# Kernel optimization log

Hardware: AMD Instinct MI355X
Metric: run time of the kernel (lower is better)

Reference implementation:

```python
import jax, jax.numpy as jnp
import numpy as np

NUM_VARS = 64
LAG = 16
H1 = 64
H2 = 1024
NUM_OUT = 1
BATCH = 16384


def setup_inputs() -> dict:
    key = jax.random.key(0)
    ks = jax.random.split(key, 8)

    def xavier(k, shape, fan_in, fan_out):
        std = float(np.sqrt(2.0 / (fan_in + fan_out)))
        return jax.random.normal(k, shape, dtype=jnp.float32) * std

    inputs = jax.random.normal(ks[0], (BATCH, NUM_VARS * LAG), dtype=jnp.float32)
    # Per-variable sub-network weights, batched over the variable axis.
    W1 = xavier(ks[1], (NUM_VARS, LAG, H1), LAG, H1)
    b1 = jnp.full((NUM_VARS, H1), 0.1, dtype=jnp.float32)
    W2 = xavier(ks[2], (NUM_VARS, H1, H1), H1, H1)
    b2 = jnp.full((NUM_VARS, H1), 0.1, dtype=jnp.float32)
    imp = (jnp.ones((NUM_VARS,), dtype=jnp.float32) / NUM_VARS
           + 1e-5 * jax.random.normal(ks[3], (NUM_VARS,), dtype=jnp.float32))
    W3 = xavier(ks[4], (NUM_VARS * H1, H2), NUM_VARS * H1, H2)
    b3 = jnp.full((H2,), 0.1, dtype=jnp.float32)
    W4 = xavier(ks[5], (H2, NUM_OUT), H2, NUM_OUT)
    b4 = jnp.full((NUM_OUT,), 0.1, dtype=jnp.float32)
    return {"inputs": inputs, "W1": W1, "b1": b1, "W2": W2, "b2": b2,
            "imp": imp, "W3": W3, "b3": b3, "W4": W4, "b4": b4}


def reference(inputs, W1, b1, W2, b2, imp, W3, b3, W4, b4):
    B = inputs.shape[0]
    # [B, V*lag] -> [B, V, lag]; slicing inputs[:, lag*i:lag*(i+1)] == x[:, i, :]
    x = inputs.reshape(B, NUM_VARS, LAG)
    # dp = 0.0 -> dropout is identity
    h = jax.nn.relu(jnp.einsum('bvl,vlh->bvh', x, W1) + b1[None])      # [B, V, H1]
    h = jax.nn.relu(jnp.einsum('bvh,vhk->bvk', h, W2) + b2[None])      # [B, V, H1]
    agg = (h * imp[None, :, None]).reshape(B, NUM_VARS * H1)            # weighted concat
    pred = jax.nn.relu(agg @ W3 + b3) @ W4 + b4                        # [B, NUM_OUT]
    return pred
```

## Files before the change

kernel.cpp:

```cpp
#include <hip/hip_runtime.h>
#include <hip/hip_bf16.h>
#include <stdint.h>

#define B_ROWS 16384
#define NVARS 64
#define LAG 16
#define H1 64
#define H2 1024
#define KDIM (NVARS * H1)

typedef __attribute__((ext_vector_type(8))) short short8;
typedef __attribute__((ext_vector_type(4))) short short4v;
typedef __attribute__((ext_vector_type(4))) float f32x4;

typedef __attribute__((address_space(3))) uint8_t lds_u8;
typedef const __attribute__((address_space(1))) uint8_t glob_u8;

__device__ __forceinline__ void gload_lds16(const void* g, void* l) {
    __builtin_amdgcn_global_load_lds((glob_u8*)g, (lds_u8*)l, 16, 0, 0);
}

__device__ __forceinline__ short f2bf_s(float x) {
    __hip_bfloat16 h = __float2bfloat16(x);
    return *(short*)&h;
}
__device__ __forceinline__ float bf_s2f(short s) {
    __hip_bfloat16 h = *(__hip_bfloat16*)&s;
    return __bfloat162float(h);
}

__global__ __launch_bounds__(256) void prep_w12_kernel(
    const float* __restrict__ W1, const float* __restrict__ W2,
    short* __restrict__ w1bh, short* __restrict__ w1bl,
    short* __restrict__ w2bh, short* __restrict__ w2bl) {
    const int v = blockIdx.x, t = threadIdx.x;
    for (int idx = t; idx < 64 * 32; idx += 256) {
        int col = idx >> 5, k = idx & 31;
        float wv = W1[((size_t)v * LAG + (k & 15)) * H1 + col];
        short hi = f2bf_s(wv);
        w1bh[((size_t)v * 64 + col) * 40 + k] = hi;
        w1bl[((size_t)v * 64 + col) * 40 + k] = (k < 16) ? f2bf_s(wv - bf_s2f(hi)) : (short)0;
    }
    for (int idx = t; idx < 64 * 64; idx += 256) {
        int col = idx >> 6, k = idx & 63;
        float wv = W2[((size_t)v * H1 + k) * H1 + col];
        short hi = f2bf_s(wv);
        w2bh[((size_t)v * 64 + col) * 72 + k] = hi;
        w2bl[((size_t)v * 64 + col) * 72 + k] = f2bf_s(wv - bf_s2f(hi));
    }
}

__global__ __launch_bounds__(256) void subnets_fused_kernel(
    const float* __restrict__ inputs, const float* __restrict__ b1g,
    const float* __restrict__ b2g, const float* __restrict__ impg,
    const short* __restrict__ w1bh_g, const short* __restrict__ w1bl_g,
    const short* __restrict__ w2bh_g, const short* __restrict__ w2bl_g,
    const float* __restrict__ w3, const float* __restrict__ b4,
    __hip_bfloat16* __restrict__ w3t, float* __restrict__ out,
    __hip_bfloat16* __restrict__ agg) {
    __shared__ __align__(16) char smem[38912];
    const int bid = blockIdx.x;
    const int t = threadIdx.x;

    if (bid < 1024) {
        float (*tile)[65] = (float (*)[65])smem;
        const int k0 = (bid >> 4) * 64;
        const int n0 = (bid & 15) * 64;
        const int c = t & 63, r0 = t >> 6;
#pragma unroll
        for (int i = 0; i < 16; i++) {
            int r = r0 + i * 4;
            tile[r][c] = w3[(size_t)(k0 + r) * H2 + n0 + c];
        }
        __syncthreads();
#pragma unroll
        for (int i = 0; i < 16; i++) {
            int nr = r0 + i * 4;
            w3t[(size_t)(n0 + nr) * KDIM + k0 + c] = __float2bfloat16(tile[c][nr]);
        }
        return;
    }
    if (bid < 1088) {
        out[(bid - 1024) * 256 + t] = b4[0];
        return;
    }

    const int sbid = bid - 1088;
    const int v = sbid >> 7;
    const int b0 = (sbid & 127) * 128;
    const int lane = t & 63, wv = t >> 6;
    const int l15 = lane & 15, g = lane >> 4;

    short* xsS   = (short*)smem;
    short* w1bhS = (short*)(smem + 10240);
    short* w1blS = (short*)(smem + 15360);
    short* Hs    = (short*)smem;
    short* w2bhS = (short*)(smem + 20480);
    short* w2blS = (short*)(smem + 29696);

    for (int c = t; c < 320; c += 256) {
        gload_lds16(w1bh_g + (size_t)v * 2560 + c * 8, (char*)w1bhS + c * 16);
        gload_lds16(w1bl_g + (size_t)v * 2560 + c * 8, (char*)w1blS + c * 16);
    }
    for (int c = t; c < 576; c += 256) {
        gload_lds16(w2bh_g + (size_t)v * 4608 + c * 8, (char*)w2bhS + c * 16);
        gload_lds16(w2bl_g + (size_t)v * 4608 + c * 8, (char*)w2blS + c * 16);
    }
#pragma unroll
    for (int i = 0; i < 2; i++) {
        int idx = t + i * 256;
        int row = idx >> 2, seg = idx & 3;
        float4 x4 = *(const float4*)(inputs + (size_t)(b0 + row) * (NVARS * LAG) + v * LAG + seg * 4);
        const float* xp = (const float*)&x4;
        short4v hv, lv;
#pragma unroll
        for (int j = 0; j < 4; j++) {
            short hi = f2bf_s(xp[j]);
            hv[j] = hi;
            lv[j] = f2bf_s(xp[j] - bf_s2f(hi));
        }
        *(short4v*)&xsS[row * 40 + seg * 4] = hv;
        *(short4v*)&xsS[row * 40 + 16 + seg * 4] = lv;
    }
    __syncthreads();

    short8 a1[2], b1hF[4], b1lF[4];
#pragma unroll
    for (int mt = 0; mt < 2; mt++)
        a1[mt] = *(const short8*)&xsS[(wv * 32 + mt * 16 + l15) * 40 + g * 8];
#pragma unroll
    for (int nt = 0; nt < 4; nt++) {
        b1hF[nt] = *(const short8*)&w1bhS[(nt * 16 + l15) * 40 + g * 8];
        b1lF[nt] = *(const short8*)&w1blS[(nt * 16 + l15) * 40 + g * 8];
    }
    f32x4 acc1[2][4];
#pragma unroll
    for (int mt = 0; mt < 2; mt++)
#pragma unroll
        for (int nt = 0; nt < 4; nt++) {
            acc1[mt][nt] = (f32x4){0.f, 0.f, 0.f, 0.f};
            acc1[mt][nt] = __builtin_amdgcn_mfma_f32_16x16x32_bf16(a1[mt], b1hF[nt], acc1[mt][nt], 0, 0, 0);
            acc1[mt][nt] = __builtin_amdgcn_mfma_f32_16x16x32_bf16(a1[mt], b1lF[nt], acc1[mt][nt], 0, 0, 0);
        }
    __syncthreads();

#pragma unroll
    for (int mt = 0; mt < 2; mt++)
#pragma unroll
        for (int nt = 0; nt < 4; nt++) {
            int col = nt * 16 + l15;
            float bias = b1g[v * H1 + col];
#pragma unroll
            for (int r = 0; r < 4; r++) {
                float h = fmaxf(acc1[mt][nt][r] + bias, 0.f);
                int row = wv * 32 + mt * 16 + g * 4 + r;
                Hs[row * 72 + col] = f2bf_s(h);
            }
        }
    __syncthreads();

    short8 a2[2][2], b2hF[4][2], b2lF[4][2];
#pragma unroll
    for (int mt = 0; mt < 2; mt++)
#pragma unroll
        for (int kc = 0; kc < 2; kc++)
            a2[mt][kc] = *(const short8*)&Hs[(wv * 32 + mt * 16 + l15) * 72 + kc * 32 + g * 8];
#pragma unroll
    for (int nt = 0; nt < 4; nt++)
#pragma unroll
        for (int kc = 0; kc < 2; kc++) {
            b2hF[nt][kc] = *(const short8*)&w2bhS[(nt * 16 + l15) * 72 + kc * 32 + g * 8];
            b2lF[nt][kc] = *(const short8*)&w2blS[(nt * 16 + l15) * 72 + kc * 32 + g * 8];
        }
    f32x4 acc2[2][4];
#pragma unroll
    for (int mt = 0; mt < 2; mt++)
#pragma unroll
        for (int nt = 0; nt < 4; nt++) {
            f32x4 a = (f32x4){0.f, 0.f, 0.f, 0.f};
            a = __builtin_amdgcn_mfma_f32_16x16x32_bf16(a2[mt][0], b2hF[nt][0], a, 0, 0, 0);
            a = __builtin_amdgcn_mfma_f32_16x16x32_bf16(a2[mt][1], b2hF[nt][1], a, 0, 0, 0);
            a = __builtin_amdgcn_mfma_f32_16x16x32_bf16(a2[mt][0], b2lF[nt][0], a, 0, 0, 0);
            a = __builtin_amdgcn_mfma_f32_16x16x32_bf16(a2[mt][1], b2lF[nt][1], a, 0, 0, 0);
            acc2[mt][nt] = a;
        }

    const float impv = impg[v];
#pragma unroll
    for (int mt = 0; mt < 2; mt++)
#pragma unroll
        for (int nt = 0; nt < 4; nt++) {
            int col = nt * 16 + l15;
            float bias = b2g[v * H1 + col];
#pragma unroll
            for (int r = 0; r < 4; r++) {
                float o = fmaxf(acc2[mt][nt][r] + bias, 0.f) * impv;
                int row = b0 + wv * 32 + mt * 16 + g * 4 + r;
                agg[(size_t)row * KDIM + v * H1 + col] = __float2bfloat16(o);
            }
        }
}

#define NT 128

__global__ __launch_bounds__(512, 4) void gemm3_kernel(
    const __hip_bfloat16* __restrict__ agg,
    const __hip_bfloat16* __restrict__ w3t,
    const float* __restrict__ b3, const float* __restrict__ W4,
    float* __restrict__ out) {
    const int bid = ((blockIdx.x & 7) << 6) + (blockIdx.x >> 3);
    const int brow = (bid >> 2) * 128;
    const int bcol = (bid & 3) * 256;
    const int t = threadIdx.x;
    const int lane = t & 63;
    const int wid = t >> 6;
    const int wm = wid >> 2, wn = wid & 3;
    const int l15 = lane & 15, g = lane >> 4;

    __shared__ __align__(16) char smem[73728];

    const int rA = t >> 2;
    const int colA = ((t & 3) * 8) ^ ((rA & 8) ? 16 : 0);
    const int cB0 = t, cB1 = t + 512;
    const int rB0 = cB0 >> 2, rB1 = cB1 >> 2;
    const int colB0 = ((cB0 & 3) * 8) ^ ((rB0 & 8) ? 16 : 0);
    const int colB1 = ((cB1 & 3) * 8) ^ ((rB1 & 8) ? 16 : 0);
    const __hip_bfloat16* aS = agg + (size_t)(brow + rA) * KDIM + colA;
    const __hip_bfloat16* bS0 = w3t + (size_t)(bcol + rB0) * KDIM + colB0;
    const __hip_bfloat16* bS1 = w3t + (size_t)(bcol + rB1) * KDIM + colB1;

#define STAGE(p, kt) do { \
        gload_lds16(aS + (size_t)(kt) * 32,  smem + (p) * 24576 + t * 16); \
        gload_lds16(bS0 + (size_t)(kt) * 32, smem + (p) * 24576 + 8192 + cB0 * 16); \
        gload_lds16(bS1 + (size_t)(kt) * 32, smem + (p) * 24576 + 8192 + cB1 * 16); } while (0)

    const int coff = (g * 16) ^ ((l15 & 8) ? 32 : 0);
    const int aBase = (wm * 64 + l15) * 64 + coff;
    const int bBase = 8192 + (wn * 64 + l15) * 64 + coff;

#define LDFRAGS(p) do { \
        fa[0] = *(const short8*)(smem + (p) * 24576 + aBase + 0 * 1024); \
        fa[1] = *(const short8*)(smem + (p) * 24576 + aBase + 1 * 1024); \
        fa[2] = *(const short8*)(smem + (p) * 24576 + aBase + 2 * 1024); \
        fa[3] = *(const short8*)(smem + (p) * 24576 + aBase + 3 * 1024); \
        fb[0] = *(const short8*)(smem + (p) * 24576 + bBase + 0 * 1024); \
        fb[1] = *(const short8*)(smem + (p) * 24576 + bBase + 1 * 1024); \
        fb[2] = *(const short8*)(smem + (p) * 24576 + bBase + 2 * 1024); \
        fb[3] = *(const short8*)(smem + (p) * 24576 + bBase + 3 * 1024); } while (0)

#define MM() do { \
        __builtin_amdgcn_s_setprio(1); \
        _Pragma("unroll") \
        for (int mm = 0; mm < 4; mm++) \
            _Pragma("unroll") \
            for (int nn = 0; nn < 4; nn++) \
                acc[mm][nn] = __builtin_amdgcn_mfma_f32_16x16x32_bf16( \
                    fa[mm], fb[nn], acc[mm][nn], 0, 0, 0); \
        __builtin_amdgcn_s_setprio(0); } while (0)

#define TILE(p, DOSTAGE, ps, kts, VMSTR) do { \
        if (DOSTAGE) STAGE(ps, kts); \
        LDFRAGS(p); \
        MM(); \
        asm volatile(VMSTR ::: "memory"); \
        __builtin_amdgcn_s_barrier(); \
        __builtin_amdgcn_sched_barrier(0); } while (0)

    short8 fa[4], fb[4];
    f32x4 acc[4][4];
#pragma unroll
    for (int m = 0; m < 4; m++)
#pragma unroll
        for (int n = 0; n < 4; n++) acc[m][n] = (f32x4){0.f, 0.f, 0.f, 0.f};

    STAGE(0, 0);
    STAGE(1, 1);
    asm volatile("s_waitcnt vmcnt(3)" ::: "memory");
    __builtin_amdgcn_s_barrier();
    __builtin_amdgcn_sched_barrier(0);

    for (int i = 0; i < 42; ++i) {
        const int tt = i * 3;
        TILE(0, 1, 2, tt + 2, "s_waitcnt vmcnt(3)");
        TILE(1, 1, 0, tt + 3, "s_waitcnt vmcnt(3)");
        TILE(2, 1, 1, tt + 4, "s_waitcnt vmcnt(3)");
    }
    TILE(0, 0, 0, 0, "s_waitcnt vmcnt(0)");
    LDFRAGS(1);
    MM();

    float bias[4], w4v[4];
#pragma unroll
    for (int n = 0; n < 4; n++) {
        int col = bcol + wn * 64 + n * 16 + l15;
        bias[n] = b3[col];
        w4v[n] = W4[col];
    }
#pragma unroll
    for (int m = 0; m < 4; m++) {
        float pr0 = 0.f, pr1 = 0.f, pr2 = 0.f, pr3 = 0.f;
#pragma unroll
        for (int n = 0; n < 4; n++) {
            pr0 += fmaxf(acc[m][n][0] + bias[n], 0.f) * w4v[n];
            pr1 += fmaxf(acc[m][n][1] + bias[n], 0.f) * w4v[n];
            pr2 += fmaxf(acc[m][n][2] + bias[n], 0.f) * w4v[n];
            pr3 += fmaxf(acc[m][n][3] + bias[n], 0.f) * w4v[n];
        }
#pragma unroll
        for (int mask = 1; mask < 16; mask <<= 1) {
            pr0 += __shfl_xor(pr0, mask, 64);
            pr1 += __shfl_xor(pr1, mask, 64);
            pr2 += __shfl_xor(pr2, mask, 64);
            pr3 += __shfl_xor(pr3, mask, 64);
        }
        if (l15 == 0) {
            int row = brow + wm * 64 + m * 16 + g * 4;
            atomicAdd(&out[row + 0], pr0);
            atomicAdd(&out[row + 1], pr1);
            atomicAdd(&out[row + 2], pr2);
            atomicAdd(&out[row + 3], pr3);
        }
    }
}

extern "C" void kernel_launch(void* const* d_in, const int* in_sizes, int n_in,
                              void* d_out, int out_size, void* d_ws, size_t ws_size,
                              hipStream_t stream) {
    const float* inputs = (const float*)d_in[0];
    const float* W1 = (const float*)d_in[1];
    const float* b1 = (const float*)d_in[2];
    const float* W2 = (const float*)d_in[3];
    const float* b2 = (const float*)d_in[4];
    const float* imp = (const float*)d_in[5];
    const float* W3 = (const float*)d_in[6];
    const float* b3 = (const float*)d_in[7];
    const float* W4 = (const float*)d_in[8];
    const float* b4 = (const float*)d_in[9];
    float* out = (float*)d_out;

    char* ws = (char*)d_ws;
    const size_t agg_bytes = (size_t)B_ROWS * KDIM * 2;
    const size_t w3t_bytes = (size_t)H2 * KDIM * 2;
    const size_t w1b_bytes = (size_t)NVARS * 64 * 40 * 2;
    const size_t w2b_bytes = (size_t)NVARS * 64 * 72 * 2;

    __hip_bfloat16* agg = (__hip_bfloat16*)ws;
    __hip_bfloat16* w3t = (__hip_bfloat16*)(ws + agg_bytes);
    short* w1bh = (short*)(ws + agg_bytes + w3t_bytes);
    short* w1bl = (short*)(ws + agg_bytes + w3t_bytes + w1b_bytes);
    short* w2bh = (short*)(ws + agg_bytes + w3t_bytes + 2 * w1b_bytes);
    short* w2bl = (short*)(ws + agg_bytes + w3t_bytes + 2 * w1b_bytes + w2b_bytes);

    hipLaunchKernelGGL(prep_w12_kernel, dim3(NVARS), dim3(256), 0, stream,
                       W1, W2, w1bh, w1bl, w2bh, w2bl);
    hipLaunchKernelGGL(subnets_fused_kernel, dim3(1088 + NVARS * (B_ROWS / 128)), dim3(256), 0, stream,
                       inputs, b1, b2, imp, w1bh, w1bl, w2bh, w2bl,
                       W3, b4, w3t, out, agg);
    hipLaunchKernelGGL(gemm3_kernel, dim3((B_ROWS / 128) * (H2 / 256)), dim3(512), 0, stream,
                       agg, w3t, b3, W4, out);
}
```

Measured before the change: 186.7 us.

## Enlarge GEMM3 tile to 256x256 with 1024 threads and 4-stage LDS pipeline

The final large GEMM now uses 1024-thread blocks computing 256x256 output tiles instead of 128x256, which halves the number of blocks and raises operand reuse per block. The LDS ring buffer grows from three to four stages, and fragment loads are issued before the next stage's global-to-LDS copy. The aim is to cut redundant global traffic for W3 and hide more memory latency. In exchange it needs 128 KB of LDS per block, which limits occupancy to one block per CU. It also leaves 256 blocks for the whole GPU, which may underfill the machine and hurt tail balance.

Result: faster. 166.0 us (-11.1%).

```diff
diff --git a/kernel.cpp b/kernel.cpp
--- a/kernel.cpp
+++ b/kernel.cpp
@@ -203,13 +203,13 @@
 
 #define NT 128
 
-__global__ __launch_bounds__(512, 4) void gemm3_kernel(
+__global__ __launch_bounds__(1024, 4) void gemm3_kernel(
     const __hip_bfloat16* __restrict__ agg,
     const __hip_bfloat16* __restrict__ w3t,
     const float* __restrict__ b3, const float* __restrict__ W4,
     float* __restrict__ out) {
-    const int bid = ((blockIdx.x & 7) << 6) + (blockIdx.x >> 3);
-    const int brow = (bid >> 2) * 128;
+    const int bid = ((blockIdx.x & 7) << 5) + (blockIdx.x >> 3);
+    const int brow = (bid >> 2) * 256;
     const int bcol = (bid & 3) * 256;
     const int t = threadIdx.x;
     const int lane = t & 63;
@@ -217,38 +217,35 @@
     const int wm = wid >> 2, wn = wid & 3;
     const int l15 = lane & 15, g = lane >> 4;
 
-    __shared__ __align__(16) char smem[73728];
+    __shared__ __align__(16) char smem[131072];
 
     const int rA = t >> 2;
     const int colA = ((t & 3) * 8) ^ ((rA & 8) ? 16 : 0);
-    const int cB0 = t, cB1 = t + 512;
-    const int rB0 = cB0 >> 2, rB1 = cB1 >> 2;
-    const int colB0 = ((cB0 & 3) * 8) ^ ((rB0 & 8) ? 16 : 0);
-    const int colB1 = ((cB1 & 3) * 8) ^ ((rB1 & 8) ? 16 : 0);
     const __hip_bfloat16* aS = agg + (size_t)(brow + rA) * KDIM + colA;
-    const __hip_bfloat16* bS0 = w3t + (size_t)(bcol + rB0) * KDIM + colB0;
-    const __hip_bfloat16* bS1 = w3t + (size_t)(bcol + rB1) * KDIM + colB1;
+    const __hip_bfloat16* bS = w3t + (size_t)(bcol + rA) * KDIM + colA;
 
 #define STAGE(p, kt) do { \
-        gload_lds16(aS + (size_t)(kt) * 32,  smem + (p) * 24576 + t * 16); \
-        gload_lds16(bS0 + (size_t)(kt) * 32, smem + (p) * 24576 + 8192 + cB0 * 16); \
-        gload_lds16(bS1 + (size_t)(kt) * 32, smem + (p) * 24576 + 8192 + cB1 * 16); } while (0)
+        gload_lds16(aS + (size_t)(kt) * 32, smem + (p) * 32768 + t * 16); \
+        gload_lds16(bS + (size_t)(kt) * 32, smem + (p) * 32768 + 16384 + t * 16); } while (0)
 
     const int coff = (g * 16) ^ ((l15 & 8) ? 32 : 0);
     const int aBase = (wm * 64 + l15) * 64 + coff;
-    const int bBase = 8192 + (wn * 64 + l15) * 64 + coff;
-
-#define LDFRAGS(p) do { \
-        fa[0] = *(const short8*)(smem + (p) * 24576 + aBase + 0 * 1024); \
-        fa[1] = *(const short8*)(smem + (p) * 24576 + aBase + 1 * 1024); \
-        fa[2] = *(const short8*)(smem + (p) * 24576 + aBase + 2 * 1024); \
-        fa[3] = *(const short8*)(smem + (p) * 24576 + aBase + 3 * 1024); \
-        fb[0] = *(const short8*)(smem + (p) * 24576 + bBase + 0 * 1024); \
-        fb[1] = *(const short8*)(smem + (p) * 24576 + bBase + 1 * 1024); \
-        fb[2] = *(const short8*)(smem + (p) * 24576 + bBase + 2 * 1024); \
-        fb[3] = *(const short8*)(smem + (p) * 24576 + bBase + 3 * 1024); } while (0)
-
-#define MM() do { \
+    const int bBase = 16384 + (wn * 64 + l15) * 64 + coff;
+
+#define LDA(i, p) fa[i] = *(const short8*)(smem + (p) * 32768 + aBase + (i) * 1024)
+#define LDB(i, p) fb[i] = *(const short8*)(smem + (p) * 32768 + bBase + (i) * 1024)
+
+    short8 fa[4], fb[4];
+    f32x4 acc[4][4];
+#pragma unroll
+    for (int m = 0; m < 4; m++)
+#pragma unroll
+        for (int n = 0; n < 4; n++) acc[m][n] = (f32x4){0.f, 0.f, 0.f, 0.f};
+
+#define TILE(p, DOSTAGE, kt3, VMSTR) do { \
+        LDA(0, p); LDA(1, p); LDA(2, p); LDA(3, p); \
+        LDB(0, p); LDB(1, p); LDB(2, p); LDB(3, p); \
+        if (DOSTAGE) STAGE((kt3) & 3, kt3); \
         __builtin_amdgcn_s_setprio(1); \
         _Pragma("unroll") \
         for (int mm = 0; mm < 4; mm++) \
@@ -256,38 +253,35 @@
             for (int nn = 0; nn < 4; nn++) \
                 acc[mm][nn] = __builtin_amdgcn_mfma_f32_16x16x32_bf16( \
                     fa[mm], fb[nn], acc[mm][nn], 0, 0, 0); \
-        __builtin_amdgcn_s_setprio(0); } while (0)
-
-#define TILE(p, DOSTAGE, ps, kts, VMSTR) do { \
-        if (DOSTAGE) STAGE(ps, kts); \
-        LDFRAGS(p); \
-        MM(); \
+        __builtin_amdgcn_s_setprio(0); \
         asm volatile(VMSTR ::: "memory"); \
         __builtin_amdgcn_s_barrier(); \
         __builtin_amdgcn_sched_barrier(0); } while (0)
 
-    short8 fa[4], fb[4];
-    f32x4 acc[4][4];
-#pragma unroll
-    for (int m = 0; m < 4; m++)
-#pragma unroll
-        for (int n = 0; n < 4; n++) acc[m][n] = (f32x4){0.f, 0.f, 0.f, 0.f};
-
     STAGE(0, 0);
     STAGE(1, 1);
-    asm volatile("s_waitcnt vmcnt(3)" ::: "memory");
+    STAGE(2, 2);
+    asm volatile("s_waitcnt vmcnt(4)" ::: "memory");
     __builtin_amdgcn_s_barrier();
     __builtin_amdgcn_sched_barrier(0);
 
-    for (int i = 0; i < 42; ++i) {
-        const int tt = i * 3;
-        TILE(0, 1, 2, tt + 2, "s_waitcnt vmcnt(3)");
-        TILE(1, 1, 0, tt + 3, "s_waitcnt vmcnt(3)");
-        TILE(2, 1, 1, tt + 4, "s_waitcnt vmcnt(3)");
-    }
-    TILE(0, 0, 0, 0, "s_waitcnt vmcnt(0)");
-    LDFRAGS(1);
-    MM();
+#pragma unroll 4
+    for (int tt = 0; tt < NT - 4; ++tt) {
+        TILE(tt & 3, 1, tt + 3, "s_waitcnt vmcnt(4)");
+    }
+    TILE(0, 1, 127, "s_waitcnt vmcnt(4)");
+    TILE(1, 0, 0,   "s_waitcnt vmcnt(2)");
+    TILE(2, 0, 0,   "s_waitcnt vmcnt(0)");
+    LDA(0, 3); LDA(1, 3); LDA(2, 3); LDA(3, 3);
+    LDB(0, 3); LDB(1, 3); LDB(2, 3); LDB(3, 3);
+    __builtin_amdgcn_s_setprio(1);
+#pragma unroll
+    for (int mm = 0; mm < 4; mm++)
+#pragma unroll
+        for (int nn = 0; nn < 4; nn++)
+            acc[mm][nn] = __builtin_amdgcn_mfma_f32_16x16x32_bf16(
+                fa[mm], fb[nn], acc[mm][nn], 0, 0, 0);
+    __builtin_amdgcn_s_setprio(0);
 
     float bias[4], w4v[4];
 #pragma unroll
@@ -356,6 +350,6 @@
     hipLaunchKernelGGL(subnets_fused_kernel, dim3(1088 + NVARS * (B_ROWS / 128)), dim3(256), 0, stream,
                        inputs, b1, b2, imp, w1bh, w1bl, w2bh, w2bl,
                        W3, b4, w3t, out, agg);
-    hipLaunchKernelGGL(gemm3_kernel, dim3((B_ROWS / 128) * (H2 / 256)), dim3(512), 0, stream,
+    hipLaunchKernelGGL(gemm3_kernel, dim3((B_ROWS / 256) * (H2 / 256)), dim3(1024), 0, stream,
                        agg, w3t, b3, W4, out);
 }
```
